# Kernel tuning notes

Measured on AMD Instinct MI355X. Metric: run time of the kernel, lower is better.

## Reference

```python
import jax, jax.numpy as jnp
import numpy as np
from jax import lax

B, S, D_MODEL, H, P = 16, 2048, 512, 8, 128
DEPTH = D_MODEL // H          # 64
C = (S + P - 1) // P          # chunk_size = 16


def _build_table():
    # table[R-1, c, :] = indices of positions assigned to cluster c when R real tokens,
    # padded with R (the padded zero-row index when R == S, else first pad position).
    table = np.zeros((S, P, C), dtype=np.int32)
    cols = np.arange(C)
    for R in range(1, S + 1):
        assign = np.minimum(np.arange(R) * P // R, P - 1)  # nondecreasing
        starts = np.searchsorted(assign, np.arange(P), side='left')
        ends = np.searchsorted(assign, np.arange(P), side='right')
        cand = starts[:, None] + cols[None, :]
        table[R - 1] = np.where(cand < ends[:, None], cand, R)
    return table


def setup_inputs() -> dict:
    key = jax.random.key(0)
    ks = jax.random.split(key, 12)
    def glorot(k, shp):
        fan = shp[-2] + shp[-1]
        return jax.random.normal(k, shp, jnp.float32) * np.sqrt(2.0 / fan).astype(np.float32)
    x = jax.random.normal(ks[0], (B, S, D_MODEL), jnp.float32)
    lengths = jax.random.randint(ks[1], (B,), S // 2, S + 1)
    mask = jnp.arange(S)[None, :] < lengths[:, None]
    return dict(
        x=x, mask=mask,
        wq=glorot(ks[2], (D_MODEL, D_MODEL)),
        wk=glorot(ks[3], (D_MODEL, D_MODEL)),
        wv=glorot(ks[4], (D_MODEL, D_MODEL)),
        e_w=glorot(ks[5], (H, P, C)),
        f_w=glorot(ks[6], (H, P, C)),
        ck1=glorot(ks[7], (1, P, 1, 1)), cb1=jnp.zeros((1,), jnp.float32),
        ck3=glorot(ks[8], (3, P, 1, 1)), cb3=jnp.zeros((1,), jnp.float32),
        ck5=glorot(ks[9], (5, P, 1, 1)), cb5=jnp.zeros((1,), jnp.float32),
        dw=glorot(ks[10], (D_MODEL, D_MODEL)),
        db=jnp.zeros((D_MODEL,), jnp.float32),
        table=jnp.asarray(_build_table()),
    )


def _conv_same(z, kern, bias):
    # z: (N, S, P, 1), kern: (h, P, 1, 1); Keras Conv2D padding='same', stride 1
    return lax.conv_general_dilated(
        z, kern, window_strides=(1, 1), padding='SAME',
        dimension_numbers=('NHWC', 'HWIO', 'NHWC')) + bias


def _forward(x, mask, wq, wk, wv, e_w, f_w, ck1, cb1, ck3, cb3, ck5, cb5, dw, db, table):
    b = x.shape[0]
    split = lambda t: t.reshape(b, S, H, DEPTH).transpose(0, 2, 1, 3)  # (B,H,S,depth)
    q = split(x @ wq)
    k = split(x @ wk)
    v = split(x @ wv)
    pad = ((0, 0), (0, 0), (0, 1), (0, 0))
    k = jnp.pad(k, pad)  # (B,H,S+1,depth) zero pad row at index S
    v = jnp.pad(v, pad)
    real_counts = jnp.clip(jnp.sum(mask.astype(jnp.int32), axis=1), 1, S)
    pos = table[real_counts - 1]                  # (B,P,C) per-batch cluster index table
    gather = jax.vmap(lambda t, idx: t[:, idx])   # gather over seq axis per batch
    k_ch = gather(k, pos)                          # (B,H,P,C,depth)
    v_ch = gather(v, pos)
    k_proj = jnp.einsum('bhpcd,hpc->bhpd', k_ch, e_w)
    v_proj = jnp.einsum('bhpcd,hpc->bhpd', v_ch, f_w)
    scores = jnp.einsum('bhsd,bhpd->bhsp', q, k_proj) / jnp.sqrt(jnp.float32(DEPTH))
    z = scores.reshape(b * H, S, P, 1)
    # mean of the three conv branches (filter heights 1,3,5)
    conv_avg = (_conv_same(z, ck1, cb1) + _conv_same(z, ck3, cb3) + _conv_same(z, ck5, cb5)) / 3.0
    scores = conv_avg.reshape(b, H, S, P)
    w = jax.nn.softmax(scores, axis=-1)
    attn = jnp.einsum('bhsp,bhpd->bhsd', w, v_proj)
    concat = attn.transpose(0, 2, 1, 3).reshape(b, S, D_MODEL)
    return concat @ dw + db


def reference(x, mask, wq, wk, wv, e_w, f_w, ck1, cb1, ck3, cb3, ck5, cb5, dw, db, table):
    return _forward(x, mask, wq, wk, wv, e_w, f_w, ck1, cb1, ck3, cb3, ck5, cb5, dw, db, table)
```

## Files before the change

### kernel.cpp

```cpp
#include <hip/hip_runtime.h>
#include <hip/hip_bf16.h>

#define BN 16
#define SN 2048
#define DM 512
#define HN 8
#define PN 128
#define DEPTH 64
#define CSZ 16

typedef unsigned short u16;
typedef __bf16 bf16x8 __attribute__((ext_vector_type(8)));
typedef float f32x4 __attribute__((ext_vector_type(4)));

#define OFF_QB   0ull
#define OFF_KB   8388608ull
#define OFF_VB   16777216ull
#define OFF_CB   25165824ull
#define OFF_WQT  33554432ull
#define OFF_WKT  33685504ull
#define OFF_WVT  33816576ull
#define OFF_DWT  33947648ull
#define OFF_KP   34078720ull
#define OFF_VPT  35127296ull
#define OFF_KEP  35651584ull
#define OFF_EFF  38273024ull
#define OFF_CNT  38273664ull

__device__ __forceinline__ u16 f2bf(float f) {
    unsigned u = __float_as_uint(f);
    u = (u + 0x7fffu + ((u >> 16) & 1u)) >> 16;
    return (u16)u;
}
__device__ __forceinline__ float b2f(u16 h) {
    return __uint_as_float(((unsigned)h) << 16);
}

__device__ __forceinline__ void xcd_decode(int bid, int nmem, int& g, int& j) {
    int xcd = bid & 7;
    int t = bid >> 3;
    j = t % nmem;
    g = (t / nmem) * 8 + xcd;
}

__global__ void count_kernel(const void* mask, int* counts) {
    __shared__ int red[256];
    int b = blockIdx.x, tid = threadIdx.x;
    const unsigned char* mb = (const unsigned char*)mask;
    bool is_byte = (mb[1] != 0);
    int local = 0;
    if (is_byte) {
        const unsigned char* row = mb + (size_t)b * SN;
        for (int s = tid; s < SN; s += 256) local += (row[s] != 0);
    } else {
        const int* row = (const int*)mask + (size_t)b * SN;
        for (int s = tid; s < SN; s += 256) local += (row[s] != 0);
    }
    red[tid] = local;
    __syncthreads();
    for (int st = 128; st > 0; st >>= 1) {
        if (tid < st) red[tid] += red[tid + st];
        __syncthreads();
    }
    if (tid == 0) {
        int c = red[0];
        if (c < 1) c = 1;
        if (c > SN) c = SN;
        counts[b] = c;
    }
}

__global__ void eff_kernel(const float* ck1, const float* ck3, const float* ck5, float* eff) {
    int i = threadIdx.x;
    if (i < 640) {
        int t = i >> 7, j = i & 127;
        float v = ck5[t * 128 + j];
        if (t >= 1 && t <= 3) v += ck3[(t - 1) * 128 + j];
        if (t == 2) v += ck1[j];
        eff[i] = v * (1.0f / 3.0f);
    }
}

__global__ void convert_wT_kernel(const float* w0, const float* w1, const float* w2, const float* w3,
                                  u16* o0, u16* o1, u16* o2, u16* o3) {
    int z = blockIdx.z;
    const float* W = (z == 0) ? w0 : (z == 1) ? w1 : (z == 2) ? w2 : w3;
    u16* O = (z == 0) ? o0 : (z == 1) ? o1 : (z == 2) ? o2 : o3;
    __shared__ float t[32][33];
    int k0 = blockIdx.y * 32, n0 = blockIdx.x * 32;
    int lx = threadIdx.x & 31, ly = threadIdx.x >> 5;
#pragma unroll
    for (int i = 0; i < 4; i++) t[ly + i * 8][lx] = W[(size_t)(k0 + ly + i * 8) * 512 + n0 + lx];
    __syncthreads();
#pragma unroll
    for (int i = 0; i < 4; i++) O[(size_t)(n0 + ly + i * 8) * 512 + k0 + lx] = f2bf(t[lx][ly + i * 8]);
}

__global__ __launch_bounds__(512, 2) void gemm_qkv(const float* __restrict__ X,
                                                   const u16* __restrict__ WT,
                                                   u16* __restrict__ Q,
                                                   u16* __restrict__ K,
                                                   u16* __restrict__ V) {
    __shared__ __align__(16) char smem[40960];
    char* AsB = smem;

    int g, j;
    xcd_decode(blockIdx.x, 8, g, j);
    const int m0 = g * 128, n0 = j * 64;
    const int tid = threadIdx.x;
    const int w = tid >> 6, l = tid & 63;
    const int wm = w >> 2, wn = w & 3;
    const int cl = l & 15, kg = l >> 4;

    f32x4 acc[3][4];
    const f32x4 z4 = {0.f, 0.f, 0.f, 0.f};
#pragma unroll
    for (int z = 0; z < 3; z++)
#pragma unroll
        for (int mf = 0; mf < 4; mf++) acc[z][mf] = z4;

    for (int kt = 0; kt < 8; kt++) {
        __syncthreads();
#pragma unroll
        for (int it = 0; it < 2; it++) {
            int i = it * 512 + tid;
            int row = i >> 3, slot = i & 7;
            const float* src = X + (size_t)(m0 + row) * 512 + kt * 64 + ((slot ^ (row & 7)) * 8);
            float4 v0 = *(const float4*)src;
            float4 v1 = *(const float4*)(src + 4);
            int4 pk;
            pk.x = (int)(f2bf(v0.x) | ((unsigned)f2bf(v0.y) << 16));
            pk.y = (int)(f2bf(v0.z) | ((unsigned)f2bf(v0.w) << 16));
            pk.z = (int)(f2bf(v1.x) | ((unsigned)f2bf(v1.y) << 16));
            pk.w = (int)(f2bf(v1.z) | ((unsigned)f2bf(v1.w) << 16));
            *(int4*)(AsB + row * 128 + slot * 16) = pk;
        }
#pragma unroll
        for (int z = 0; z < 3; z++) {
            int row = tid >> 3, slot = tid & 7;
            const char* src = (const char*)(WT + (size_t)z * 262144 +
                                            (size_t)(n0 + row) * 512 + kt * 64 + ((slot ^ (row & 7)) * 8));
            __builtin_amdgcn_global_load_lds((const __attribute__((address_space(1))) void*)src,
                                             (__attribute__((address_space(3))) void*)(smem + 16384 + z * 8192 + tid * 16),
                                             16, 0, 0);
        }
        __syncthreads();
#pragma unroll
        for (int ks = 0; ks < 2; ks++) {
            int slot = ks * 4 + kg;
            bf16x8 a[4];
#pragma unroll
            for (int mf = 0; mf < 4; mf++) {
                int row = wm * 64 + mf * 16 + cl;
                a[mf] = *(const bf16x8*)(AsB + row * 128 + ((slot ^ (row & 7)) * 16));
            }
#pragma unroll
            for (int z = 0; z < 3; z++) {
                const char* Bz = smem + 16384 + z * 8192;
                int brow = wn * 16 + cl;
                bf16x8 b = *(const bf16x8*)(Bz + brow * 128 + ((slot ^ (brow & 7)) * 16));
#pragma unroll
                for (int mf = 0; mf < 4; mf++)
                    acc[z][mf] = __builtin_amdgcn_mfma_f32_16x16x32_bf16(a[mf], b, acc[z][mf], 0, 0, 0);
            }
        }
    }

    const int rl = l >> 4;
    u16* Ob[3] = {Q, K, V};
#pragma unroll
    for (int z = 0; z < 3; z++)
#pragma unroll
        for (int mf = 0; mf < 4; mf++) {
            f32x4 v = acc[z][mf];
            int n = n0 + wn * 16 + cl;
            int h = n >> 6, d = n & 63;
#pragma unroll
            for (int r = 0; r < 4; r++) {
                int m = m0 + wm * 64 + mf * 16 + rl * 4 + r;
                int b = m >> 11, s = m & 2047;
                Ob[z][(size_t)((b * HN + h) * SN + s) * DEPTH + d] = f2bf(v[r]);
            }
        }
}

__global__ __launch_bounds__(256) void gemm_out(const u16* __restrict__ A,
                                                const u16* __restrict__ WT,
                                                float* __restrict__ O,
                                                const float* __restrict__ bias) {
    __shared__ __align__(16) char smem[32768];
    char* AsB = smem;
    char* BsB = smem + 16384;

    int g, j;
    xcd_decode(blockIdx.x, 4, g, j);
    const int m0 = g * 128, n0 = j * 128;
    const int tid = threadIdx.x;
    const int w = tid >> 6, l = tid & 63;
    const int wm = w >> 1, wn = w & 1;
    const int lr = l >> 3, sp = l & 7;
    const int slog = sp ^ lr;
    const int cl = l & 15, kg = l >> 4;

    const char* Ab = (const char*)A;
    const char* Bb = (const char*)WT;

    f32x4 acc[4][4];
    const f32x4 z4 = {0.f, 0.f, 0.f, 0.f};
#pragma unroll
    for (int mf = 0; mf < 4; mf++)
#pragma unroll
        for (int nf = 0; nf < 4; nf++) acc[mf][nf] = z4;

    for (int kt = 0; kt < 8; kt++) {
        __syncthreads();
#pragma unroll
        for (int i = 0; i < 4; i++) {
            int c = w * 4 + i;
            const char* ga = Ab + (size_t)(m0 + c * 8 + lr) * 1024 + kt * 128 + slog * 16;
            __builtin_amdgcn_global_load_lds((const __attribute__((address_space(1))) void*)ga,
                                             (__attribute__((address_space(3))) void*)(AsB + c * 1024),
                                             16, 0, 0);
            const char* gb = Bb + (size_t)(n0 + c * 8 + lr) * 1024 + kt * 128 + slog * 16;
            __builtin_amdgcn_global_load_lds((const __attribute__((address_space(1))) void*)gb,
                                             (__attribute__((address_space(3))) void*)(BsB + c * 1024),
                                             16, 0, 0);
        }
        __syncthreads();
#pragma unroll
        for (int ks = 0; ks < 2; ks++) {
            bf16x8 a[4], b[4];
#pragma unroll
            for (int mf = 0; mf < 4; mf++) {
                int row = wm * 64 + mf * 16 + cl;
                a[mf] = *(const bf16x8*)(AsB + row * 128 + (((ks * 4 + kg) ^ (row & 7)) * 16));
            }
#pragma unroll
            for (int nf = 0; nf < 4; nf++) {
                int row = wn * 64 + nf * 16 + cl;
                b[nf] = *(const bf16x8*)(BsB + row * 128 + (((ks * 4 + kg) ^ (row & 7)) * 16));
            }
#pragma unroll
            for (int mf = 0; mf < 4; mf++)
#pragma unroll
                for (int nf = 0; nf < 4; nf++)
                    acc[mf][nf] = __builtin_amdgcn_mfma_f32_16x16x32_bf16(a[mf], b[nf], acc[mf][nf], 0, 0, 0);
        }
    }

    const int rl = l >> 4;
#pragma unroll
    for (int mf = 0; mf < 4; mf++)
#pragma unroll
        for (int nf = 0; nf < 4; nf++) {
            f32x4 v = acc[mf][nf];
            int n = n0 + wn * 64 + nf * 16 + cl;
            float bs = bias[n];
#pragma unroll
            for (int r = 0; r < 4; r++) {
                int m = m0 + wm * 64 + mf * 16 + rl * 4 + r;
                O[(size_t)m * 512 + n] = v[r] + bs;
            }
        }
}

__global__ void kvproj_kernel(const u16* __restrict__ Kin, const u16* __restrict__ Vin,
                              const int* __restrict__ table, const int* __restrict__ counts,
                              const float* __restrict__ e_w, const float* __restrict__ f_w,
                              float* __restrict__ kproj, u16* __restrict__ vpT) {
    int p = blockIdx.x;
    int b = blockIdx.y;
    int tid = threadIdx.x;
    int h = tid >> 6, d = tid & 63;
    __shared__ int poss[16];
    __shared__ float ew_s[8][16], fw_s[8][16];
    if (tid < 16) {
        int R = counts[b];
        poss[tid] = table[(size_t)(R - 1) * PN * CSZ + p * CSZ + tid];
    } else if (tid >= 64 && tid < 192) {
        int t2 = tid - 64;
        ew_s[t2 >> 4][t2 & 15] = e_w[(size_t)((t2 >> 4) * PN + p) * CSZ + (t2 & 15)];
    } else if (tid >= 192 && tid < 320) {
        int t2 = tid - 192;
        fw_s[t2 >> 4][t2 & 15] = f_w[(size_t)((t2 >> 4) * PN + p) * CSZ + (t2 & 15)];
    }
    __syncthreads();
    float ka = 0.f, va = 0.f;
    size_t base = (size_t)(b * HN + h) * SN * DEPTH + d;
#pragma unroll
    for (int c = 0; c < CSZ; c++) {
        int idx = poss[c];
        if (idx < SN) {
            float kv = b2f(Kin[base + (size_t)idx * DEPTH]);
            float vv = b2f(Vin[base + (size_t)idx * DEPTH]);
            ka = fmaf(ew_s[h][c], kv, ka);
            va = fmaf(fw_s[h][c], vv, va);
        }
    }
    int bh = b * HN + h;
    kproj[((size_t)bh * PN + p) * DEPTH + d] = ka;
    vpT[(size_t)bh * 8192 + d * 128 + p] = f2bf(va);
}

__global__ __launch_bounds__(256) void ke_kernel(const float* __restrict__ kproj,
                                                 const float* __restrict__ eff,
                                                 u16* __restrict__ keP) {
    int blk = blockIdx.x;
    int bh = blk >> 1;
    int dh = (blk & 1) * 32;
    int tid = threadIdx.x;
    int p = tid & 127;
    int sub = (tid >> 7) * 16;

    __shared__ float kpad[256 * 48];
    __shared__ float ef[640];

    for (int i = tid; i < 256 * 48; i += 256) kpad[i] = 0.f;
    for (int i = tid; i < 640; i += 256) ef[i] = eff[i];
    __syncthreads();
    for (int i = tid; i < 128 * 8; i += 256) {
        int row = i >> 3, c4 = (i & 7) * 4;
        float4 v = *(const float4*)&kproj[(size_t)bh * 8192 + row * 64 + dh + c4];
        *(float4*)&kpad[(64 + row) * 48 + c4] = v;
    }
    __syncthreads();

    float4 acc[5][4];
#pragma unroll
    for (int t = 0; t < 5; t++)
#pragma unroll
        for (int i = 0; i < 4; i++) acc[t][i] = make_float4(0.f, 0.f, 0.f, 0.f);

    for (int j = 0; j < 128; j++) {
        int rr = p + j + 1;
        float4 kv[4];
#pragma unroll
        for (int i = 0; i < 4; i++) kv[i] = *(const float4*)&kpad[rr * 48 + sub + i * 4];
        float w[5];
#pragma unroll
        for (int t = 0; t < 5; t++) w[t] = ef[t * 128 + j];
#pragma unroll
        for (int t = 0; t < 5; t++)
#pragma unroll
            for (int i = 0; i < 4; i++) {
                acc[t][i].x = fmaf(w[t], kv[i].x, acc[t][i].x);
                acc[t][i].y = fmaf(w[t], kv[i].y, acc[t][i].y);
                acc[t][i].z = fmaf(w[t], kv[i].z, acc[t][i].z);
                acc[t][i].w = fmaf(w[t], kv[i].w, acc[t][i].w);
            }
    }

    size_t obase = (size_t)bh * 40960 + (size_t)p * 320;
#pragma unroll
    for (int t = 0; t < 5; t++)
#pragma unroll
        for (int i = 0; i < 4; i++) {
            int d0 = dh + sub + i * 4;
            ushort4 o;
            o.x = f2bf(acc[t][i].x * 0.125f);
            o.y = f2bf(acc[t][i].y * 0.125f);
            o.z = f2bf(acc[t][i].z * 0.125f);
            o.w = f2bf(acc[t][i].w * 0.125f);
            *(ushort4*)&keP[obase + t * 64 + d0] = o;
        }
}

__global__ __launch_bounds__(256) void attn_kernel(const u16* __restrict__ qg,
                                                   const u16* __restrict__ keP,
                                                   const u16* __restrict__ vpT,
                                                   u16* __restrict__ concat) {
    __shared__ __align__(16) char smem[32768];
    char* qswz = smem;
    char* keB = smem + 8704;
    char* wlds = smem;
    char* vps = smem + 16384;

    int bh, st;
    xcd_decode(blockIdx.x, 32, bh, st);
    const int b = bh >> 3, h = bh & 7;
    const int s0 = st * 64;
    const int tid = threadIdx.x;
    const int w = tid >> 6, l = tid & 63;
    const int cl = l & 15, kg = l >> 4;

    const u16* qb = qg + (size_t)bh * SN * DEPTH;
    for (int i = tid; i < 68 * 8; i += 256) {
        int row = i >> 3, slot = i & 7;
        int srow = s0 + row - 2;
        int4 val = make_int4(0, 0, 0, 0);
        if (srow >= 0 && srow < SN)
            val = *(const int4*)(qb + (size_t)srow * 64 + slot * 8);
        *(int4*)(qswz + row * 128 + ((slot ^ (row & 7)) * 16)) = val;
    }

    f32x4 acc[8];
    const f32x4 z4 = {0.f, 0.f, 0.f, 0.f};
#pragma unroll
    for (int nf = 0; nf < 8; nf++) acc[nf] = z4;

    const char* kePb = (const char*)(keP + (size_t)bh * 40960);
    for (int kt = 0; kt < 5; kt++) {
        __syncthreads();
#pragma unroll
        for (int it = 0; it < 4; it++) {
            int i = it * 256 + tid;
            int p = i >> 3, slot = i & 7;
            const char* src = kePb + 2 * ((size_t)p * 320 + kt * 64) + ((slot ^ (p & 7)) * 16);
            __builtin_amdgcn_global_load_lds((const __attribute__((address_space(1))) void*)src,
                                             (__attribute__((address_space(3))) void*)(keB + i * 16),
                                             16, 0, 0);
        }
        __syncthreads();
#pragma unroll
        for (int ks = 0; ks < 2; ks++) {
            int slot = ks * 4 + kg;
            int arow = w * 16 + kt + cl;
            bf16x8 af = *(const bf16x8*)(qswz + arow * 128 + ((slot ^ (arow & 7)) * 16));
#pragma unroll
            for (int nf = 0; nf < 8; nf++) {
                int prow = nf * 16 + cl;
                bf16x8 bf = *(const bf16x8*)(keB + prow * 128 + ((slot ^ (prow & 7)) * 16));
                acc[nf] = __builtin_amdgcn_mfma_f32_16x16x32_bf16(af, bf, acc[nf], 0, 0, 0);
            }
        }
    }
    __syncthreads();

    const char* vpb = (const char*)(vpT + (size_t)bh * 8192);
#pragma unroll
    for (int it = 0; it < 4; it++) {
        int i = it * 256 + tid;
        int d = i >> 4, slot = i & 15;
        const char* src = vpb + 2 * ((size_t)d * 128) + ((slot ^ (d & 7)) * 16);
        __builtin_amdgcn_global_load_lds((const __attribute__((address_space(1))) void*)src,
                                         (__attribute__((address_space(3))) void*)(vps + i * 16),
                                         16, 0, 0);
    }

    float inv[4];
#pragma unroll
    for (int r = 0; r < 4; r++) {
        float m = acc[0][r];
#pragma unroll
        for (int nf = 1; nf < 8; nf++) m = fmaxf(m, acc[nf][r]);
        m = fmaxf(m, __shfl_xor(m, 1));
        m = fmaxf(m, __shfl_xor(m, 2));
        m = fmaxf(m, __shfl_xor(m, 4));
        m = fmaxf(m, __shfl_xor(m, 8));
        float s = 0.f;
#pragma unroll
        for (int nf = 0; nf < 8; nf++) {
            float e = __expf(acc[nf][r] - m);
            acc[nf][r] = e;
            s += e;
        }
        s += __shfl_xor(s, 1);
        s += __shfl_xor(s, 2);
        s += __shfl_xor(s, 4);
        s += __shfl_xor(s, 8);
        inv[r] = 1.0f / s;
    }
#pragma unroll
    for (int r = 0; r < 4; r++) {
        int row = w * 16 + kg * 4 + r;
#pragma unroll
        for (int nf = 0; nf < 8; nf++) {
            int col = nf * 16 + cl;
            int slot = col >> 3, within = col & 7;
            *(u16*)(wlds + row * 256 + ((slot ^ (row & 7)) * 8 + within) * 2) = f2bf(acc[nf][r] * inv[r]);
        }
    }
    __syncthreads();

    f32x4 acc2[4];
#pragma unroll
    for (int nf = 0; nf < 4; nf++) acc2[nf] = z4;
#pragma unroll
    for (int ks = 0; ks < 4; ks++) {
        int slot = ks * 4 + kg;
        int arow = w * 16 + cl;
        bf16x8 af = *(const bf16x8*)(wlds + arow * 256 + ((slot ^ (arow & 7)) * 16));
#pragma unroll
        for (int nf = 0; nf < 4; nf++) {
            int drow = nf * 16 + cl;
            bf16x8 bf = *(const bf16x8*)(vps + drow * 256 + ((slot ^ (drow & 7)) * 16));
            acc2[nf] = __builtin_amdgcn_mfma_f32_16x16x32_bf16(af, bf, acc2[nf], 0, 0, 0);
        }
    }
#pragma unroll
    for (int nf = 0; nf < 4; nf++) {
#pragma unroll
        for (int r = 0; r < 4; r++) {
            int srow = s0 + w * 16 + kg * 4 + r;
            int d = nf * 16 + cl;
            concat[((size_t)b * SN + srow) * DM + h * 64 + d] = f2bf(acc2[nf][r]);
        }
    }
}

extern "C" void kernel_launch(void* const* d_in, const int* in_sizes, int n_in,
                              void* d_out, int out_size, void* d_ws, size_t ws_size,
                              hipStream_t stream) {
    const float* x = (const float*)d_in[0];
    const void* mask = d_in[1];
    const float* wq = (const float*)d_in[2];
    const float* wk = (const float*)d_in[3];
    const float* wv = (const float*)d_in[4];
    const float* e_w = (const float*)d_in[5];
    const float* f_w = (const float*)d_in[6];
    const float* ck1 = (const float*)d_in[7];
    const float* ck3 = (const float*)d_in[9];
    const float* ck5 = (const float*)d_in[11];
    const float* dw = (const float*)d_in[13];
    const float* db = (const float*)d_in[14];
    const int* table = (const int*)d_in[15];

    float* ws = (float*)d_ws;
    u16* qb = (u16*)(ws + OFF_QB);
    u16* kb = (u16*)(ws + OFF_KB);
    u16* vb = (u16*)(ws + OFF_VB);
    u16* cb = (u16*)(ws + OFF_CB);
    u16* wqT = (u16*)(ws + OFF_WQT);
    u16* wkT = (u16*)(ws + OFF_WKT);
    u16* wvT = (u16*)(ws + OFF_WVT);
    u16* dwT = (u16*)(ws + OFF_DWT);
    float* kp = ws + OFF_KP;
    u16* vpT = (u16*)(ws + OFF_VPT);
    u16* keP = (u16*)(ws + OFF_KEP);
    float* eff = ws + OFF_EFF;
    int* counts = (int*)(ws + OFF_CNT);
    float* out = (float*)d_out;

    count_kernel<<<dim3(16), dim3(256), 0, stream>>>(mask, counts);
    eff_kernel<<<dim3(1), dim3(640), 0, stream>>>(ck1, ck3, ck5, eff);
    convert_wT_kernel<<<dim3(16, 16, 4), dim3(256), 0, stream>>>(wq, wk, wv, dw, wqT, wkT, wvT, dwT);
    gemm_qkv<<<dim3(2048), dim3(512), 0, stream>>>(x, wqT, qb, kb, vb);
    kvproj_kernel<<<dim3(128, 16), dim3(512), 0, stream>>>(kb, vb, table, counts, e_w, f_w, kp, vpT);
    ke_kernel<<<dim3(256), dim3(256), 0, stream>>>(kp, eff, keP);
    attn_kernel<<<dim3(4096), dim3(256), 0, stream>>>(qb, keP, vpT, cb);
    gemm_out<<<dim3(1024), dim3(256), 0, stream>>>(cb, dwT, out, db);
}
```

Baseline: 247.8 us.

## Double-buffer QKV GEMM shared memory to overlap global loads with MFMA

The QKV projection GEMM now uses two shared-memory stages: the next K-tile of X is loaded into registers and the next weight tile is issued via global_load_lds while MFMAs run on the current tile. The X tile is packed to bf16 and stored after the compute, which removes one barrier per iteration. Shared memory doubles to 80KB and launch bounds drop to one block per CU, which lowers occupancy. The float-to-bf16 conversion also switches to the compiler's native __bf16 cast.

```diff
diff --git a/kernel.cpp b/kernel.cpp
--- a/kernel.cpp
+++ b/kernel.cpp
@@ -35,6 +35,21 @@
 __device__ __forceinline__ float b2f(u16 h) {
     return __uint_as_float(((unsigned)h) << 16);
 }
+__device__ __forceinline__ unsigned pk2bf(float x, float y) {
+    __bf16 ha = (__bf16)x, hb = (__bf16)y;
+    u16 a, b;
+    __builtin_memcpy(&a, &ha, 2);
+    __builtin_memcpy(&b, &hb, 2);
+    return (unsigned)a | ((unsigned)b << 16);
+}
+__device__ __forceinline__ int4 pack8(float4 u, float4 v) {
+    int4 p;
+    p.x = (int)pk2bf(u.x, u.y);
+    p.y = (int)pk2bf(u.z, u.w);
+    p.z = (int)pk2bf(v.x, v.y);
+    p.w = (int)pk2bf(v.z, v.w);
+    return p;
+}
 
 __device__ __forceinline__ void xcd_decode(int bid, int nmem, int& g, int& j) {
     int xcd = bid & 7;
@@ -96,13 +111,12 @@
     for (int i = 0; i < 4; i++) O[(size_t)(n0 + ly + i * 8) * 512 + k0 + lx] = f2bf(t[lx][ly + i * 8]);
 }
 
-__global__ __launch_bounds__(512, 2) void gemm_qkv(const float* __restrict__ X,
+__global__ __launch_bounds__(512, 1) void gemm_qkv(const float* __restrict__ X,
                                                    const u16* __restrict__ WT,
                                                    u16* __restrict__ Q,
                                                    u16* __restrict__ K,
                                                    u16* __restrict__ V) {
-    __shared__ __align__(16) char smem[40960];
-    char* AsB = smem;
+    __shared__ __align__(16) char smem[81920];
 
     int g, j;
     xcd_decode(blockIdx.x, 8, g, j);
@@ -112,6 +126,14 @@
     const int wm = w >> 2, wn = w & 3;
     const int cl = l & 15, kg = l >> 4;
 
+    const int r0 = tid >> 3, slot = tid & 7;
+    const float* xb0 = X + (size_t)(m0 + r0) * 512 + ((slot ^ (r0 & 7)) * 8);
+    const float* xb1 = X + (size_t)(m0 + 64 + r0) * 512 + ((slot ^ (r0 & 7)) * 8);
+    const char* wsrc = (const char*)(WT + (size_t)(n0 + r0) * 512 + ((slot ^ (r0 & 7)) * 8));
+
+    char* pc = smem;
+    char* pn = smem + 40960;
+
     f32x4 acc[3][4];
     const f32x4 z4 = {0.f, 0.f, 0.f, 0.f};
 #pragma unroll
@@ -119,51 +141,58 @@
 #pragma unroll
         for (int mf = 0; mf < 4; mf++) acc[z][mf] = z4;
 
+    float4 a0, a1, a2, a3;
+    a0 = *(const float4*)(xb0);
+    a1 = *(const float4*)(xb0 + 4);
+    a2 = *(const float4*)(xb1);
+    a3 = *(const float4*)(xb1 + 4);
+#pragma unroll
+    for (int z = 0; z < 3; z++)
+        __builtin_amdgcn_global_load_lds((const __attribute__((address_space(1))) void*)(wsrc + (size_t)z * 524288),
+                                         (__attribute__((address_space(3))) void*)(pc + 16384 + z * 8192 + tid * 16),
+                                         16, 0, 0);
+    *(int4*)(pc + r0 * 128 + slot * 16) = pack8(a0, a1);
+    *(int4*)(pc + (64 + r0) * 128 + slot * 16) = pack8(a2, a3);
+    __syncthreads();
+
     for (int kt = 0; kt < 8; kt++) {
-        __syncthreads();
-#pragma unroll
-        for (int it = 0; it < 2; it++) {
-            int i = it * 512 + tid;
-            int row = i >> 3, slot = i & 7;
-            const float* src = X + (size_t)(m0 + row) * 512 + kt * 64 + ((slot ^ (row & 7)) * 8);
-            float4 v0 = *(const float4*)src;
-            float4 v1 = *(const float4*)(src + 4);
-            int4 pk;
-            pk.x = (int)(f2bf(v0.x) | ((unsigned)f2bf(v0.y) << 16));
-            pk.y = (int)(f2bf(v0.z) | ((unsigned)f2bf(v0.w) << 16));
-            pk.z = (int)(f2bf(v1.x) | ((unsigned)f2bf(v1.y) << 16));
-            pk.w = (int)(f2bf(v1.z) | ((unsigned)f2bf(v1.w) << 16));
-            *(int4*)(AsB + row * 128 + slot * 16) = pk;
-        }
-#pragma unroll
-        for (int z = 0; z < 3; z++) {
-            int row = tid >> 3, slot = tid & 7;
-            const char* src = (const char*)(WT + (size_t)z * 262144 +
-                                            (size_t)(n0 + row) * 512 + kt * 64 + ((slot ^ (row & 7)) * 8));
-            __builtin_amdgcn_global_load_lds((const __attribute__((address_space(1))) void*)src,
-                                             (__attribute__((address_space(3))) void*)(smem + 16384 + z * 8192 + tid * 16),
-                                             16, 0, 0);
-        }
-        __syncthreads();
+        if (kt < 7) {
+            const float* s0 = xb0 + (kt + 1) * 64;
+            const float* s1 = xb1 + (kt + 1) * 64;
+            a0 = *(const float4*)(s0);
+            a1 = *(const float4*)(s0 + 4);
+            a2 = *(const float4*)(s1);
+            a3 = *(const float4*)(s1 + 4);
+#pragma unroll
+            for (int z = 0; z < 3; z++)
+                __builtin_amdgcn_global_load_lds((const __attribute__((address_space(1))) void*)(wsrc + (size_t)z * 524288 + (size_t)(kt + 1) * 128),
+                                                 (__attribute__((address_space(3))) void*)(pn + 16384 + z * 8192 + tid * 16),
+                                                 16, 0, 0);
+        }
 #pragma unroll
         for (int ks = 0; ks < 2; ks++) {
-            int slot = ks * 4 + kg;
+            int sl = ks * 4 + kg;
             bf16x8 a[4];
 #pragma unroll
             for (int mf = 0; mf < 4; mf++) {
                 int row = wm * 64 + mf * 16 + cl;
-                a[mf] = *(const bf16x8*)(AsB + row * 128 + ((slot ^ (row & 7)) * 16));
+                a[mf] = *(const bf16x8*)(pc + row * 128 + ((sl ^ (row & 7)) * 16));
             }
 #pragma unroll
             for (int z = 0; z < 3; z++) {
-                const char* Bz = smem + 16384 + z * 8192;
                 int brow = wn * 16 + cl;
-                bf16x8 b = *(const bf16x8*)(Bz + brow * 128 + ((slot ^ (brow & 7)) * 16));
+                bf16x8 b = *(const bf16x8*)(pc + 16384 + z * 8192 + brow * 128 + ((sl ^ (brow & 7)) * 16));
 #pragma unroll
                 for (int mf = 0; mf < 4; mf++)
                     acc[z][mf] = __builtin_amdgcn_mfma_f32_16x16x32_bf16(a[mf], b, acc[z][mf], 0, 0, 0);
             }
         }
+        if (kt < 7) {
+            *(int4*)(pn + r0 * 128 + slot * 16) = pack8(a0, a1);
+            *(int4*)(pn + (64 + r0) * 128 + slot * 16) = pack8(a2, a3);
+        }
+        __syncthreads();
+        char* t = pc; pc = pn; pn = t;
     }
 
     const int rl = l >> 4;
```

New measurement: 243.0 us. About the same (-1.9%).

## Retile QKV GEMM to 128x128 per-projection tiles with 256 threads

Applied to the files above, without the earlier changes.

The QKV projection GEMM is retiled so that each block computes a 128x128 output tile of a single projection (Q, K or V) with 4 waves, instead of 128x64 tiles across all three projections with 8 waves. Each wave now does a 4x4 MFMA fragment grid, which gives more reuse of each LDS read. The fp32 X loads are batched before the bf16 pack, and packing uses the hardware bf16 conversion. The trade-off is that the fp32 X tile is now re-read and re-converted three times (once per projection), and the grid grows to 3072 blocks.

```diff
diff --git a/kernel.cpp b/kernel.cpp
--- a/kernel.cpp
+++ b/kernel.cpp
@@ -35,6 +35,21 @@
 __device__ __forceinline__ float b2f(u16 h) {
     return __uint_as_float(((unsigned)h) << 16);
 }
+__device__ __forceinline__ unsigned pk2bf(float x, float y) {
+    __bf16 ha = (__bf16)x, hb = (__bf16)y;
+    u16 a, b;
+    __builtin_memcpy(&a, &ha, 2);
+    __builtin_memcpy(&b, &hb, 2);
+    return (unsigned)a | ((unsigned)b << 16);
+}
+__device__ __forceinline__ int4 pack8(float4 u, float4 v) {
+    int4 p;
+    p.x = (int)pk2bf(u.x, u.y);
+    p.y = (int)pk2bf(u.z, u.w);
+    p.z = (int)pk2bf(v.x, v.y);
+    p.w = (int)pk2bf(v.z, v.w);
+    return p;
+}
 
 __device__ __forceinline__ void xcd_decode(int bid, int nmem, int& g, int& j) {
     int xcd = bid & 7;
@@ -96,90 +111,98 @@
     for (int i = 0; i < 4; i++) O[(size_t)(n0 + ly + i * 8) * 512 + k0 + lx] = f2bf(t[lx][ly + i * 8]);
 }
 
-__global__ __launch_bounds__(512, 2) void gemm_qkv(const float* __restrict__ X,
-                                                   const u16* __restrict__ WT,
-                                                   u16* __restrict__ Q,
-                                                   u16* __restrict__ K,
-                                                   u16* __restrict__ V) {
-    __shared__ __align__(16) char smem[40960];
+__global__ __launch_bounds__(256) void gemm_qkv(const float* __restrict__ X,
+                                                const u16* __restrict__ WT,
+                                                u16* __restrict__ Q,
+                                                u16* __restrict__ K,
+                                                u16* __restrict__ V) {
+    __shared__ __align__(16) char smem[32768];
     char* AsB = smem;
-
-    int g, j;
-    xcd_decode(blockIdx.x, 8, g, j);
-    const int m0 = g * 128, n0 = j * 64;
+    char* BsB = smem + 16384;
+
+    int g, mem;
+    xcd_decode(blockIdx.x, 12, g, mem);
+    const int z = mem >> 2;
+    const int m0 = g * 128, n0 = (mem & 3) * 128;
     const int tid = threadIdx.x;
     const int w = tid >> 6, l = tid & 63;
-    const int wm = w >> 2, wn = w & 3;
+    const int wm = w >> 1, wn = w & 1;
+    const int lr = l >> 3, sp = l & 7;
+    const int slog = sp ^ lr;
     const int cl = l & 15, kg = l >> 4;
 
-    f32x4 acc[3][4];
+    const char* Bb = (const char*)(WT + (size_t)z * 262144);
+
+    f32x4 acc[4][4];
     const f32x4 z4 = {0.f, 0.f, 0.f, 0.f};
 #pragma unroll
-    for (int z = 0; z < 3; z++)
-#pragma unroll
-        for (int mf = 0; mf < 4; mf++) acc[z][mf] = z4;
+    for (int mf = 0; mf < 4; mf++)
+#pragma unroll
+        for (int nf = 0; nf < 4; nf++) acc[mf][nf] = z4;
 
     for (int kt = 0; kt < 8; kt++) {
         __syncthreads();
 #pragma unroll
-        for (int it = 0; it < 2; it++) {
-            int i = it * 512 + tid;
-            int row = i >> 3, slot = i & 7;
-            const float* src = X + (size_t)(m0 + row) * 512 + kt * 64 + ((slot ^ (row & 7)) * 8);
-            float4 v0 = *(const float4*)src;
-            float4 v1 = *(const float4*)(src + 4);
-            int4 pk;
-            pk.x = (int)(f2bf(v0.x) | ((unsigned)f2bf(v0.y) << 16));
-            pk.y = (int)(f2bf(v0.z) | ((unsigned)f2bf(v0.w) << 16));
-            pk.z = (int)(f2bf(v1.x) | ((unsigned)f2bf(v1.y) << 16));
-            pk.w = (int)(f2bf(v1.z) | ((unsigned)f2bf(v1.w) << 16));
-            *(int4*)(AsB + row * 128 + slot * 16) = pk;
-        }
-#pragma unroll
-        for (int z = 0; z < 3; z++) {
-            int row = tid >> 3, slot = tid & 7;
-            const char* src = (const char*)(WT + (size_t)z * 262144 +
-                                            (size_t)(n0 + row) * 512 + kt * 64 + ((slot ^ (row & 7)) * 8));
-            __builtin_amdgcn_global_load_lds((const __attribute__((address_space(1))) void*)src,
-                                             (__attribute__((address_space(3))) void*)(smem + 16384 + z * 8192 + tid * 16),
+        for (int i = 0; i < 4; i++) {
+            int c = w * 4 + i;
+            const char* gb = Bb + (size_t)(n0 + c * 8 + lr) * 1024 + kt * 128 + slog * 16;
+            __builtin_amdgcn_global_load_lds((const __attribute__((address_space(1))) void*)gb,
+                                             (__attribute__((address_space(3))) void*)(BsB + c * 1024),
                                              16, 0, 0);
         }
+        {
+            float4 av[4][2];
+#pragma unroll
+            for (int it = 0; it < 4; it++) {
+                int i = it * 256 + tid;
+                int row = i >> 3, slot = i & 7;
+                const float* src = X + (size_t)(m0 + row) * 512 + kt * 64 + ((slot ^ (row & 7)) * 8);
+                av[it][0] = *(const float4*)src;
+                av[it][1] = *(const float4*)(src + 4);
+            }
+#pragma unroll
+            for (int it = 0; it < 4; it++) {
+                int i = it * 256 + tid;
+                int row = i >> 3, slot = i & 7;
+                *(int4*)(AsB + row * 128 + slot * 16) = pack8(av[it][0], av[it][1]);
+            }
+        }
         __syncthreads();
 #pragma unroll
         for (int ks = 0; ks < 2; ks++) {
-            int slot = ks * 4 + kg;
-            bf16x8 a[4];
+            bf16x8 a[4], b[4];
 #pragma unroll
             for (int mf = 0; mf < 4; mf++) {
                 int row = wm * 64 + mf * 16 + cl;
-                a[mf] = *(const bf16x8*)(AsB + row * 128 + ((slot ^ (row & 7)) * 16));
-            }
-#pragma unroll
-            for (int z = 0; z < 3; z++) {
-                const char* Bz = smem + 16384 + z * 8192;
-                int brow = wn * 16 + cl;
-                bf16x8 b = *(const bf16x8*)(Bz + brow * 128 + ((slot ^ (brow & 7)) * 16));
-#pragma unroll
-                for (int mf = 0; mf < 4; mf++)
-                    acc[z][mf] = __builtin_amdgcn_mfma_f32_16x16x32_bf16(a[mf], b, acc[z][mf], 0, 0, 0);
-            }
+                a[mf] = *(const bf16x8*)(AsB + row * 128 + (((ks * 4 + kg) ^ (row & 7)) * 16));
+            }
+#pragma unroll
+            for (int nf = 0; nf < 4; nf++) {
+                int row = wn * 64 + nf * 16 + cl;
+                b[nf] = *(const bf16x8*)(BsB + row * 128 + (((ks * 4 + kg) ^ (row & 7)) * 16));
+            }
+#pragma unroll
+            for (int mf = 0; mf < 4; mf++)
+#pragma unroll
+                for (int nf = 0; nf < 4; nf++)
+                    acc[mf][nf] = __builtin_amdgcn_mfma_f32_16x16x32_bf16(a[mf], b[nf], acc[mf][nf], 0, 0, 0);
         }
     }
 
     const int rl = l >> 4;
-    u16* Ob[3] = {Q, K, V};
-#pragma unroll
-    for (int z = 0; z < 3; z++)
-#pragma unroll
-        for (int mf = 0; mf < 4; mf++) {
-            f32x4 v = acc[z][mf];
-            int n = n0 + wn * 16 + cl;
+    u16* Ob = (z == 0) ? Q : (z == 1) ? K : V;
+#pragma unroll
+    for (int mf = 0; mf < 4; mf++)
+#pragma unroll
+        for (int nf = 0; nf < 4; nf++) {
+            f32x4 v = acc[mf][nf];
+            int n = n0 + wn * 64 + nf * 16 + cl;
             int h = n >> 6, d = n & 63;
 #pragma unroll
             for (int r = 0; r < 4; r++) {
                 int m = m0 + wm * 64 + mf * 16 + rl * 4 + r;
                 int b = m >> 11, s = m & 2047;
-                Ob[z][(size_t)((b * HN + h) * SN + s) * DEPTH + d] = f2bf(v[r]);
+                Ob[(size_t)((b * HN + h) * SN + s) * DEPTH + d] = f2bf(v[r]);
             }
         }
 }
@@ -534,7 +557,7 @@
     count_kernel<<<dim3(16), dim3(256), 0, stream>>>(mask, counts);
     eff_kernel<<<dim3(1), dim3(640), 0, stream>>>(ck1, ck3, ck5, eff);
     convert_wT_kernel<<<dim3(16, 16, 4), dim3(256), 0, stream>>>(wq, wk, wv, dw, wqT, wkT, wvT, dwT);
-    gemm_qkv<<<dim3(2048), dim3(512), 0, stream>>>(x, wqT, qb, kb, vb);
+    gemm_qkv<<<dim3(3072), dim3(256), 0, stream>>>(x, wqT, qb, kb, vb);
     kvproj_kernel<<<dim3(128, 16), dim3(512), 0, stream>>>(kb, vb, table, counts, e_w, f_w, kp, vpT);
     ke_kernel<<<dim3(256), dim3(256), 0, stream>>>(kp, eff, keP);
     attn_kernel<<<dim3(4096), dim3(256), 0, stream>>>(qb, keP, vpT, cb);
```

Measured after the change: 254.7 us. 2.8% more time.
